# Kernel tuning notes

Hardware: AMD Instinct MI355X
Metric: run time of the kernel (lower is better)

Reference implementation:

```python
import jax, jax.numpy as jnp
import numpy as np

N = 20000      # nodes
E = 320000     # edges (before self loops)
HID = 128      # args.hidden
HEADS = 8
C1 = HID // 2  # 64, gat1 out per head -> 512 concat
C2 = HID // 4  # 32, gat2 out per head -> 256 concat
D1 = HEADS * C1  # 512
D2 = HEADS * C2  # 256
JKD = HID + D1 + D2  # 896


def _glorot(key, shape):
    fan_in, fan_out = shape[0], shape[-1]
    s = jnp.sqrt(6.0 / (fan_in + fan_out))
    return jax.random.uniform(key, shape, jnp.float32, -s, s)


def setup_inputs() -> dict:
    key = jax.random.key(0)
    ks = jax.random.split(key, 18)
    x = jax.random.normal(ks[0], (N, HID), jnp.float32)
    edge_index = jax.random.randint(ks[1], (2, E), 0, N, dtype=jnp.int32)
    return {
        "x": x,
        "edge_index": edge_index,
        # GATv2 layer 1
        "Wl1": _glorot(ks[2], (HID, D1)), "bl1": jnp.zeros((D1,), jnp.float32),
        "Wr1": _glorot(ks[3], (HID, D1)), "br1": jnp.zeros((D1,), jnp.float32),
        "att1": _glorot(ks[4], (HEADS, C1)),
        "bias1": jnp.zeros((D1,), jnp.float32),
        # GATv2 layer 2
        "Wl2": _glorot(ks[5], (D1, D2)), "bl2": jnp.zeros((D2,), jnp.float32),
        "Wr2": _glorot(ks[6], (D1, D2)), "br2": jnp.zeros((D2,), jnp.float32),
        "att2": _glorot(ks[7], (HEADS, C2)),
        "bias2": jnp.zeros((D2,), jnp.float32),
        # JK linear
        "Wjk": _glorot(ks[8], (JKD, HID)), "bjk": jnp.zeros((HID,), jnp.float32),
    }


def gatv2_layer(x, src, dst, Wl, bl, Wr, br, att, bias, n):
    """PyG GATv2Conv (concat=True, eval mode: no dropout), neg_slope=0.2."""
    H, C = att.shape
    xl = (x @ Wl + bl).reshape(n, H, C)  # source transform (messages)
    xr = (x @ Wr + br).reshape(n, H, C)  # target transform
    e = jax.nn.leaky_relu(xl[src] + xr[dst], 0.2)        # [E,H,C]
    logits = jnp.einsum('ehc,hc->eh', e, att)            # [E,H]
    # numerically stable segment softmax over incoming edges per dst node
    m = jax.ops.segment_max(logits, dst, num_segments=n) # [N,H]
    a = jnp.exp(logits - m[dst])
    denom = jax.ops.segment_sum(a, dst, num_segments=n)
    alpha = a / denom[dst]                               # [E,H]
    out = jax.ops.segment_sum(alpha[:, :, None] * xl[src], dst, num_segments=n)
    return out.reshape(n, H * C) + bias


def reference(x, edge_index, Wl1, bl1, Wr1, br1, att1, bias1,
              Wl2, bl2, Wr2, br2, att2, bias2, Wjk, bjk):
    n = x.shape[0]
    loop = jnp.arange(n, dtype=edge_index.dtype)
    src = jnp.concatenate([edge_index[0], loop])  # add self loops (PyG default)
    dst = jnp.concatenate([edge_index[1], loop])

    jk0 = x
    h1 = jax.nn.elu(gatv2_layer(x, src, dst, Wl1, bl1, Wr1, br1, att1, bias1, n))
    h2 = jax.nn.elu(gatv2_layer(h1, src, dst, Wl2, bl2, Wr2, br2, att2, bias2, n))
    jk = jnp.concatenate([jk0, h1, h2], axis=-1)  # JumpingKnowledge('cat')
    return jk @ Wjk + bjk
```

## Files before the change

kernel.cpp:

```cpp
#include <hip/hip_runtime.h>

typedef unsigned short u16;
typedef __attribute__((ext_vector_type(8))) short bf16x8;
typedef __attribute__((ext_vector_type(4))) float f32x4;

__device__ __forceinline__ float bf2f(u16 u) { return __uint_as_float(((unsigned)u) << 16); }
__device__ __forceinline__ u16 f2bf(float f) {
  unsigned u = __float_as_uint(f);
  u += 0x7fffu + ((u >> 16) & 1u);
  return (u16)(u >> 16);
}
__device__ __forceinline__ void bf2x2(unsigned w, float& lo, float& hi) {
  lo = __uint_as_float(w << 16);
  hi = __uint_as_float(w & 0xffff0000u);
}
__device__ __forceinline__ unsigned pk2(float lo, float hi) {
  return (unsigned)f2bf(lo) | ((unsigned)f2bf(hi) << 16);
}

__device__ __forceinline__ float red8(float p) {
  p += __int_as_float(__builtin_amdgcn_ds_swizzle(__float_as_int(p), 0x041F));
  p += __int_as_float(__builtin_amdgcn_ds_swizzle(__float_as_int(p), 0x081F));
  p += __int_as_float(__builtin_amdgcn_ds_swizzle(__float_as_int(p), 0x101F));
  return p;
}
__device__ __forceinline__ float red4(float p) {
  p += __int_as_float(__builtin_amdgcn_ds_swizzle(__float_as_int(p), 0x041F));
  p += __int_as_float(__builtin_amdgcn_ds_swizzle(__float_as_int(p), 0x081F));
  return p;
}

__global__ __launch_bounds__(256) void prepw_kernel(
    const float* __restrict__ x,
    const float* __restrict__ bl1, const float* __restrict__ br1,
    const float* __restrict__ bl2, const float* __restrict__ br2,
    const float* __restrict__ Wl1, const float* __restrict__ Wr1,
    const float* __restrict__ Wl2, const float* __restrict__ Wr2,
    const float* __restrict__ Wjk,
    u16* __restrict__ XH, float* __restrict__ BC1, float* __restrict__ BC2,
    int* __restrict__ cur, u16* __restrict__ Wp,
    int nx, int total, int prepBlocks)
{
  if (blockIdx.x < prepBlocks) {
    int i = blockIdx.x * 256 + threadIdx.x;
    if (i >= total) return;
    if (i < nx) { XH[i] = f2bf(x[i]); return; }
    int j = i - nx;
    if (j < 1024) { BC1[j] = (j < 512) ? bl1[j] : br1[j - 512]; return; }
    if (j < 1536) { int t = j - 1024; BC2[t] = (t < 256) ? bl2[t] : br2[t - 256]; return; }
    cur[j - 1536] = 0;
    return;
  }
  __shared__ float T[64][65];
  int t = blockIdx.x - prepBlocks;
  const float *Wa, *Wb; int Nhalf, lds, k0, n0, KsT, SUBS; size_t obase; bool split;
  if (t < 32) {
    int kt = t & 1, nt = t >> 1;
    k0 = kt * 64; n0 = nt * 64; obase = 0; KsT = 4; SUBS = 8; split = true;
    Wa = Wl1; Wb = Wr1; Nhalf = 512; lds = 512;
  } else if (t < 96) {
    int tt = t - 32; int kt = tt & 7, nt = tt >> 3;
    k0 = kt * 64; n0 = nt * 64; obase = 262144; KsT = 16; SUBS = 8; split = true;
    Wa = Wl2; Wb = Wr2; Nhalf = 256; lds = 256;
  } else {
    int tt = t - 96; int kt = tt % 14, nt = tt / 14;
    k0 = kt * 64; n0 = nt * 64; obase = 786432; KsT = 28; SUBS = 4; split = false;
    Wa = Wjk; Wb = nullptr; Nhalf = 128; lds = 128;
  }
  const int tid = threadIdx.x;
  const int lane = tid & 63, unit = tid >> 6;
  {
    int n = n0 + lane;
    const float* S = (n < Nhalf) ? Wa : Wb;
    int nn = (n < Nhalf) ? n : n - Nhalf;
#pragma unroll
    for (int r = 0; r < 16; ++r) {
      int kl = unit + 4 * r;
      T[kl][lane] = S[(size_t)(k0 + kl) * lds + nn];
    }
  }
  __syncthreads();
  const int tn = n0 >> 6;
#pragma unroll
  for (int u = 0; u < 2; ++u) {
    int c = unit * 2 + u;
    int ks_l = c >> 2, nc = c & 3;
    int ksg = (k0 >> 5) + ks_l;
    size_t ob = obase + ((size_t)(tn * KsT + ksg) * SUBS + nc) * 512 + lane * 8;
#pragma unroll
    for (int j = 0; j < 8; ++j) {
      float v = T[ks_l * 32 + (lane >> 4) * 8 + j][nc * 16 + (lane & 15)];
      u16 h = f2bf(v);
      Wp[ob + j] = h;
      if (split) Wp[ob + 2048 + j] = f2bf(v - bf2f(h));
    }
  }
}

__global__ __launch_bounds__(256) void hist_kernel(
    const int* __restrict__ ei, int E, int ET, int* __restrict__ cnt)
{
  int e = blockIdx.x * 256 + threadIdx.x;
  if (e >= ET) return;
  int d = (e < E) ? ei[E + e] : (e - E);
  atomicAdd(&cnt[d], 1);
}

__global__ __launch_bounds__(1024) void scan_kernel(
    int* __restrict__ cnt, int* __restrict__ rowptr, int n)
{
  __shared__ int wsum[16];
  __shared__ int carry;
  const int tid = threadIdx.x, lane = tid & 63, wv = tid >> 6;
  if (tid == 0) carry = 0;
  __syncthreads();
  for (int base = 0; base < n; base += 1024) {
    int i = base + tid;
    int v = (i < n) ? cnt[i] : 0;
    if (i < n) cnt[i] = 0;
    int s = v;
#pragma unroll
    for (int ofs = 1; ofs < 64; ofs <<= 1) {
      int t = __shfl_up(s, ofs);
      if (lane >= ofs) s += t;
    }
    if (lane == 63) wsum[wv] = s;
    __syncthreads();
    if (wv == 0 && lane < 16) {
      int t = wsum[lane];
#pragma unroll
      for (int ofs = 1; ofs < 16; ofs <<= 1) {
        int u = __shfl_up(t, ofs);
        if (lane >= ofs) t += u;
      }
      wsum[lane] = t;
    }
    __syncthreads();
    int waveoff = (wv == 0) ? 0 : wsum[wv - 1];
    if (i < n) rowptr[i] = carry + waveoff + s - v;
    int tot = wsum[15];
    __syncthreads();
    if (tid == 0) carry += tot;
    __syncthreads();
  }
  if (threadIdx.x == 0) rowptr[n] = carry;
}

__global__ __launch_bounds__(256) void scatter_kernel(
    const int* __restrict__ ei, int E, int ET,
    const int* __restrict__ rowptr, int* __restrict__ cur, int* __restrict__ srcs)
{
  int e = blockIdx.x * 256 + threadIdx.x;
  if (e >= ET) return;
  int s, d;
  if (e < E) { s = ei[e]; d = ei[E + e]; } else { s = e - E; d = s; }
  int pos = rowptr[d] + atomicAdd(&cur[d], 1);
  srcs[pos] = s;
}

template<int MROWS, int NW, int WPE, bool SPLIT, bool BF16OUT, int LDSU16>
__global__ __launch_bounds__(NW * 64, WPE) void gemmct_kernel(
    const u16* __restrict__ A0, int lda0, int K0,
    const u16* __restrict__ A1, int lda1, int K1,
    const u16* __restrict__ A2, int lda2, int K2,
    const u16* __restrict__ Wp, int KsT,
    int kof0, int kof1, int kof2,
    const float* __restrict__ bias,
    void* __restrict__ Cv, int ldc, int M, int N)
{
  constexpr int SUBS = SPLIT ? 8 : 4;
  __shared__ u16 ldsA[LDSU16];
  const int tid  = threadIdx.x;
  const int lane = tid & 63;
  const int wv   = tid >> 6;
  const int quad = lane >> 4;
  const int r16  = lane & 15;
  const int m0   = blockIdx.x * MROWS;

  const u16* As[3]   = {A0, A1, A2};
  const int  Ks[3]   = {K0, K1, K2};
  const int  ldas[3] = {lda0, lda1, lda2};
  const int  kofs[3] = {kof0, kof1, kof2};

  int soff[3];
  int so = 0;
#pragma unroll
  for (int s = 0; s < 3; ++s) {
    const int K = Ks[s];
    soff[s] = so;
    if (K == 0) continue;
    const int stride = K + 8;
    const int cpr = K >> 3;
    const int sh  = 32 - __clz(cpr - 1);
    const int tot = MROWS << sh;
    for (int c = tid; c < tot; c += NW * 64) {
      int row = c >> sh, kc = c & ((1 << sh) - 1);
      if (kc < cpr) {
        int sr = m0 + row; if (sr >= M) sr = M - 1;
        uint4 v = *reinterpret_cast<const uint4*>(As[s] + (size_t)sr * ldas[s] + kc * 8);
        *reinterpret_cast<uint4*>(&ldsA[so + row * stride + kc * 8]) = v;
      }
    }
    so += MROWS * stride;
  }
  __syncthreads();

  constexpr int MM = MROWS / 16;
  for (int n0w = wv * 64; n0w < N; n0w += NW * 64) {
    const int t = n0w >> 6;
    f32x4 acc[MM][4];
#pragma unroll
    for (int mm = 0; mm < MM; ++mm)
#pragma unroll
      for (int nc = 0; nc < 4; ++nc) acc[mm][nc] = (f32x4){0.f, 0.f, 0.f, 0.f};

#pragma unroll
    for (int s = 0; s < 3; ++s) {
      const int K = Ks[s];
      if (K == 0) continue;
      const int stride = K + 8;
      const int ksb = kofs[s] >> 5;
      const u16* lbase = &ldsA[soff[s] + r16 * stride + quad * 8];

#pragma unroll 2
      for (int k0 = 0; k0 < K; k0 += 32) {
        const int ks = ksb + (k0 >> 5);
        const u16* ch = Wp + (((size_t)(t * KsT + ks) * SUBS) << 9) + lane * 8;
        bf16x8 af[MM];
#pragma unroll
        for (int mm = 0; mm < MM; ++mm)
          af[mm] = *reinterpret_cast<const bf16x8*>(lbase + mm * 16 * stride + k0);
        bf16x8 whf[4], wlf[4];
#pragma unroll
        for (int nc = 0; nc < 4; ++nc) {
          whf[nc] = *reinterpret_cast<const bf16x8*>(ch + (nc << 9));
          if (SPLIT) wlf[nc] = *reinterpret_cast<const bf16x8*>(ch + ((4 + nc) << 9));
        }
#pragma unroll
        for (int mm = 0; mm < MM; ++mm)
#pragma unroll
          for (int nc = 0; nc < 4; ++nc) {
            acc[mm][nc] = __builtin_amdgcn_mfma_f32_16x16x32_bf16(whf[nc], af[mm], acc[mm][nc], 0, 0, 0);
            if (SPLIT)
              acc[mm][nc] = __builtin_amdgcn_mfma_f32_16x16x32_bf16(wlf[nc], af[mm], acc[mm][nc], 0, 0, 0);
          }
      }
    }

#pragma unroll
    for (int mm = 0; mm < MM; ++mm) {
      const int m = m0 + mm * 16 + r16;
      if (m >= M) continue;
#pragma unroll
      for (int nc = 0; nc < 4; ++nc) {
        const int n = n0w + nc * 16 + quad * 4;
        float b0 = 0.f, b1 = 0.f, b2 = 0.f, b3 = 0.f;
        if (bias) {
          float4 bv = *reinterpret_cast<const float4*>(bias + n);
          b0 = bv.x; b1 = bv.y; b2 = bv.z; b3 = bv.w;
        }
        float v0 = acc[mm][nc][0] + b0;
        float v1 = acc[mm][nc][1] + b1;
        float v2 = acc[mm][nc][2] + b2;
        float v3 = acc[mm][nc][3] + b3;
        if (BF16OUT) {
          ushort4 o = { f2bf(v0), f2bf(v1), f2bf(v2), f2bf(v3) };
          *reinterpret_cast<ushort4*>((u16*)Cv + (size_t)m * ldc + n) = o;
        } else {
          float4 o = { v0, v1, v2, v3 };
          *reinterpret_cast<float4*>((float*)Cv + (size_t)m * ldc + n) = o;
        }
      }
    }
  }
}

template<int VPL>
__device__ __forceinline__ void load_row(const u16* p, float* dst) {
  if constexpr (VPL == 8) {
    uint4 t = *reinterpret_cast<const uint4*>(p);
    bf2x2(t.x, dst[0], dst[1]); bf2x2(t.y, dst[2], dst[3]);
    bf2x2(t.z, dst[4], dst[5]); bf2x2(t.w, dst[6], dst[7]);
  } else {
    uint2 t = *reinterpret_cast<const uint2*>(p);
    bf2x2(t.x, dst[0], dst[1]); bf2x2(t.y, dst[2], dst[3]);
  }
}

__global__ __launch_bounds__(256) void gat_node1_kernel(
    const u16* __restrict__ XLR,
    const int* __restrict__ rowptr, const int* __restrict__ srcs,
    const float* __restrict__ att, const float* __restrict__ bias,
    u16* __restrict__ Hh, int Nn)
{
  constexpr int D = 512;
  constexpr int VPL = 8;
  const int lane = threadIdx.x & 63;
  const int wv  = (blockIdx.x * 256 + threadIdx.x) >> 6;
  const int nwv = (gridDim.x * 256) >> 6;

  float c1[VPL], c2[VPL], biasR[VPL];
#pragma unroll
  for (int w = 0; w < VPL; ++w) {
    float a = att[lane * VPL + w];
    c1[w] = 0.6f * a;
    c2[w] = 0.4f * a;
    biasR[w] = bias[lane * VPL + w];
  }

  for (int d = wv; d < Nn; d += nwv) {
    float xr[VPL];
    load_row<VPL>(XLR + (size_t)d * (2 * D) + D + lane * VPL, xr);

    const int jb = rowptr[d], je = rowptr[d + 1];

    float acc[VPL];
    load_row<VPL>(XLR + (size_t)srcs[jb] * (2 * D) + lane * VPL, acc);
    float p0 = 0.f;
#pragma unroll
    for (int w = 0; w < VPL; ++w) {
      float v = acc[w] + xr[w];
      p0 = fmaf(c1[w], v, fmaf(c2[w], fabsf(v), p0));
    }
    p0 = red8(p0);
    float den = 1.f;

    int j = jb + 1;
    for (; j + 5 < je; j += 6) {
      float xs[6][VPL];
      float p[6];
#pragma unroll
      for (int q = 0; q < 6; ++q)
        load_row<VPL>(XLR + (size_t)srcs[j + q] * (2 * D) + lane * VPL, xs[q]);
#pragma unroll
      for (int q = 0; q < 6; ++q) {
        float pp = 0.f;
#pragma unroll
        for (int w = 0; w < VPL; ++w) {
          float v = xs[q][w] + xr[w];
          pp = fmaf(c1[w], v, fmaf(c2[w], fabsf(v), pp));
        }
        p[q] = pp;
      }
#pragma unroll
      for (int q = 0; q < 6; ++q)
        p[q] += __int_as_float(__builtin_amdgcn_ds_swizzle(__float_as_int(p[q]), 0x041F));
#pragma unroll
      for (int q = 0; q < 6; ++q)
        p[q] += __int_as_float(__builtin_amdgcn_ds_swizzle(__float_as_int(p[q]), 0x081F));
#pragma unroll
      for (int q = 0; q < 6; ++q)
        p[q] += __int_as_float(__builtin_amdgcn_ds_swizzle(__float_as_int(p[q]), 0x101F));
      float e[6];
#pragma unroll
      for (int q = 0; q < 6; ++q) e[q] = __expf(p[q] - p0);
      den += ((e[0] + e[1]) + (e[2] + e[3])) + (e[4] + e[5]);
#pragma unroll
      for (int w = 0; w < VPL; ++w) {
        float t0 = fmaf(e[0], xs[0][w], fmaf(e[1], xs[1][w], acc[w]));
        float t1 = fmaf(e[2], xs[2][w], fmaf(e[3], xs[3][w], t0));
        acc[w] = fmaf(e[4], xs[4][w], fmaf(e[5], xs[5][w], t1));
      }
    }
    if (j + 3 < je) {
      float xs[4][VPL];
      float p[4];
#pragma unroll
      for (int q = 0; q < 4; ++q)
        load_row<VPL>(XLR + (size_t)srcs[j + q] * (2 * D) + lane * VPL, xs[q]);
#pragma unroll
      for (int q = 0; q < 4; ++q) {
        float pp = 0.f;
#pragma unroll
        for (int w = 0; w < VPL; ++w) {
          float v = xs[q][w] + xr[w];
          pp = fmaf(c1[w], v, fmaf(c2[w], fabsf(v), pp));
        }
        p[q] = pp;
      }
#pragma unroll
      for (int q = 0; q < 4; ++q)
        p[q] += __int_as_float(__builtin_amdgcn_ds_swizzle(__float_as_int(p[q]), 0x041F));
#pragma unroll
      for (int q = 0; q < 4; ++q)
        p[q] += __int_as_float(__builtin_amdgcn_ds_swizzle(__float_as_int(p[q]), 0x081F));
#pragma unroll
      for (int q = 0; q < 4; ++q)
        p[q] += __int_as_float(__builtin_amdgcn_ds_swizzle(__float_as_int(p[q]), 0x101F));
      float e[4];
#pragma unroll
      for (int q = 0; q < 4; ++q) e[q] = __expf(p[q] - p0);
      den += (e[0] + e[1]) + (e[2] + e[3]);
#pragma unroll
      for (int w = 0; w < VPL; ++w) {
        float t0 = fmaf(e[0], xs[0][w], fmaf(e[1], xs[1][w], acc[w]));
        acc[w] = fmaf(e[2], xs[2][w], fmaf(e[3], xs[3][w], t0));
      }
      j += 4;
    }
    if (j + 1 < je) {
      float xa[VPL], xb[VPL];
      load_row<VPL>(XLR + (size_t)srcs[j]     * (2 * D) + lane * VPL, xa);
      load_row<VPL>(XLR + (size_t)srcs[j + 1] * (2 * D) + lane * VPL, xb);
      float pa = 0.f, pb = 0.f;
#pragma unroll
      for (int w = 0; w < VPL; ++w) {
        float va = xa[w] + xr[w];
        float vb = xb[w] + xr[w];
        pa = fmaf(c1[w], va, fmaf(c2[w], fabsf(va), pa));
        pb = fmaf(c1[w], vb, fmaf(c2[w], fabsf(vb), pb));
      }
      pa = red8(pa); pb = red8(pb);
      const float ea = __expf(pa - p0);
      const float eb = __expf(pb - p0);
      den += ea + eb;
#pragma unroll
      for (int w = 0; w < VPL; ++w)
        acc[w] = fmaf(ea, xa[w], fmaf(eb, xb[w], acc[w]));
      j += 2;
    }
    if (j < je) {
      float xa[VPL];
      load_row<VPL>(XLR + (size_t)srcs[j] * (2 * D) + lane * VPL, xa);
      float pa = 0.f;
#pragma unroll
      for (int w = 0; w < VPL; ++w) {
        float va = xa[w] + xr[w];
        pa = fmaf(c1[w], va, fmaf(c2[w], fabsf(va), pa));
      }
      pa = red8(pa);
      const float ea = __expf(pa - p0);
      den += ea;
#pragma unroll
      for (int w = 0; w < VPL; ++w) acc[w] = fmaf(ea, xa[w], acc[w]);
    }

    const float inv = 1.f / den;
    float o[VPL];
#pragma unroll
    for (int w = 0; w < VPL; ++w) {
      float v = fmaf(acc[w], inv, biasR[w]);
      o[w] = v > 0.f ? v : (__expf(v) - 1.f);
    }
    uint4 ov = { pk2(o[0], o[1]), pk2(o[2], o[3]), pk2(o[4], o[5]), pk2(o[6], o[7]) };
    *reinterpret_cast<uint4*>(Hh + (size_t)d * D + lane * VPL) = ov;
  }
}

__global__ __launch_bounds__(256) void gat_node2_kernel(
    const u16* __restrict__ XLR,
    const int* __restrict__ rowptr, const int* __restrict__ srcs,
    const float* __restrict__ att, const float* __restrict__ bias,
    u16* __restrict__ Hh, int Nn)
{
  constexpr int D = 256;
  const int lane = threadIdx.x & 63;
  const int half = lane >> 5;
  const int l32  = lane & 31;
  const int wv  = (blockIdx.x * 256 + threadIdx.x) >> 6;
  const int nwv = (gridDim.x * 256) >> 6;

  float c1[8], c2[8], biasR[8];
#pragma unroll
  for (int w = 0; w < 8; ++w) {
    float a = att[l32 * 8 + w];
    c1[w] = 0.6f * a;
    c2[w] = 0.4f * a;
    biasR[w] = bias[l32 * 8 + w];
  }

  for (int d = wv; d < Nn; d += nwv) {
    float xr[8];
    load_row<8>(XLR + (size_t)d * (2 * D) + D + l32 * 8, xr);

    const int jb = rowptr[d], je = rowptr[d + 1];

    float acc[8];
    load_row<8>(XLR + (size_t)srcs[jb] * (2 * D) + l32 * 8, acc);
    float p0 = 0.f;
#pragma unroll
    for (int w = 0; w < 8; ++w) {
      float v = acc[w] + xr[w];
      p0 = fmaf(c1[w], v, fmaf(c2[w], fabsf(v), p0));
    }
    p0 = red4(p0);
    float den;
    if (half) {
      den = 0.f;
#pragma unroll
      for (int w = 0; w < 8; ++w) acc[w] = 0.f;
    } else {
      den = 1.f;
    }

    int j = jb + 1;
    for (; j + 7 < je; j += 8) {
      float xs[4][8];
      float p[4];
#pragma unroll
      for (int q = 0; q < 4; ++q)
        load_row<8>(XLR + (size_t)srcs[j + 2 * q + half] * (2 * D) + l32 * 8, xs[q]);
#pragma unroll
      for (int q = 0; q < 4; ++q) {
        float pp = 0.f;
#pragma unroll
        for (int w = 0; w < 8; ++w) {
          float v = xs[q][w] + xr[w];
          pp = fmaf(c1[w], v, fmaf(c2[w], fabsf(v), pp));
        }
        p[q] = pp;
      }
#pragma unroll
      for (int q = 0; q < 4; ++q)
        p[q] += __int_as_float(__builtin_amdgcn_ds_swizzle(__float_as_int(p[q]), 0x041F));
#pragma unroll
      for (int q = 0; q < 4; ++q)
        p[q] += __int_as_float(__builtin_amdgcn_ds_swizzle(__float_as_int(p[q]), 0x081F));
      float e[4];
#pragma unroll
      for (int q = 0; q < 4; ++q) e[q] = __expf(p[q] - p0);
      den += (e[0] + e[1]) + (e[2] + e[3]);
#pragma unroll
      for (int w = 0; w < 8; ++w) {
        float t0 = fmaf(e[0], xs[0][w], fmaf(e[1], xs[1][w], acc[w]));
        acc[w] = fmaf(e[2], xs[2][w], fmaf(e[3], xs[3][w], t0));
      }
    }
    for (; j < je; j += 2) {
      int jj = j + half;
      const bool valid = jj < je;
      if (!valid) jj = je - 1;
      float xa[8];
      load_row<8>(XLR + (size_t)srcs[jj] * (2 * D) + l32 * 8, xa);
      float pa = 0.f;
#pragma unroll
      for (int w = 0; w < 8; ++w) {
        float v = xa[w] + xr[w];
        pa = fmaf(c1[w], v, fmaf(c2[w], fabsf(v), pa));
      }
      pa = red4(pa);
      const float ea = valid ? __expf(pa - p0) : 0.f;
      den += ea;
#pragma unroll
      for (int w = 0; w < 8; ++w) acc[w] = fmaf(ea, xa[w], acc[w]);
    }

    den += __shfl_xor(den, 32);
#pragma unroll
    for (int w = 0; w < 8; ++w) acc[w] += __shfl_xor(acc[w], 32);

    if (half == 0) {
      const float inv = 1.f / den;
      float o[8];
#pragma unroll
      for (int w = 0; w < 8; ++w) {
        float v = fmaf(acc[w], inv, biasR[w]);
        o[w] = v > 0.f ? v : (__expf(v) - 1.f);
      }
      uint4 ov = { pk2(o[0], o[1]), pk2(o[2], o[3]), pk2(o[4], o[5]), pk2(o[6], o[7]) };
      *reinterpret_cast<uint4*>(Hh + (size_t)d * D + l32 * 8) = ov;
    }
  }
}


extern "C" void kernel_launch(void* const* d_in, const int* in_sizes, int n_in,
                              void* d_out, int out_size, void* d_ws, size_t ws_size,
                              hipStream_t stream) {
  const float* x     = (const float*)d_in[0];
  const int*   ei    = (const int*)d_in[1];
  const float* Wl1   = (const float*)d_in[2];
  const float* bl1   = (const float*)d_in[3];
  const float* Wr1   = (const float*)d_in[4];
  const float* br1   = (const float*)d_in[5];
  const float* att1  = (const float*)d_in[6];
  const float* bias1 = (const float*)d_in[7];
  const float* Wl2   = (const float*)d_in[8];
  const float* bl2   = (const float*)d_in[9];
  const float* Wr2   = (const float*)d_in[10];
  const float* br2   = (const float*)d_in[11];
  const float* att2  = (const float*)d_in[12];
  const float* bias2 = (const float*)d_in[13];
  const float* Wjk   = (const float*)d_in[14];
  const float* bjk   = (const float*)d_in[15];
  float* out = (float*)d_out;

  const int Nn = in_sizes[0] / 128;
  const int E  = in_sizes[1] / 2;
  const int ET = E + Nn;

  const size_t nx = (size_t)Nn * 128;

  const size_t oW1  = 0;
  const size_t oW2  = 262144;
  const size_t oWjk = 786432;
  const size_t npack = 901120;

  char* ws = (char*)d_ws;
  size_t off = 0;
  u16* XH = (u16*)(ws + off); off += nx * 2;
  u16* Wp = (u16*)(ws + off); off += npack * 2;
  float* BC1 = (float*)(ws + off); off += 1024 * 4;
  float* BC2 = (float*)(ws + off); off += 512 * 4;
  u16* XLR1 = (u16*)(ws + off);
  u16* XLR2 = XLR1;
  off += (size_t)Nn * 1024 * 2;
  u16* H1h = (u16*)(ws + off); off += (size_t)Nn * 512 * 2;
  u16* H2h = (u16*)(ws + off); off += (size_t)Nn * 256 * 2;
  int* rowptr = (int*)(ws + off); off += (size_t)(Nn + 1) * 4;
  int* cur    = (int*)(ws + off); off += (size_t)Nn * 4;
  int* srcs   = (int*)(ws + off); off += (size_t)ET * 4;

  const int nodeblocks = 5000;

  const int nprep = (int)(nx + 1536 + Nn);
  const int prepBlocks = (nprep + 255) / 256;
  prepw_kernel<<<prepBlocks + 124, 256, 0, stream>>>(
      x, bl1, br1, bl2, br2, Wl1, Wr1, Wl2, Wr2, Wjk,
      XH, BC1, BC2, cur, Wp, (int)nx, nprep, prepBlocks);
  hist_kernel<<<(ET + 255) / 256, 256, 0, stream>>>(ei, E, ET, cur);
  scan_kernel<<<1, 1024, 0, stream>>>(cur, rowptr, Nn);
  scatter_kernel<<<(ET + 255) / 256, 256, 0, stream>>>(ei, E, ET, rowptr, cur, srcs);

  gemmct_kernel<32, 8, 4, true, true, 32 * 136>
      <<<(Nn + 31) / 32, 512, 0, stream>>>(
      XH, 128, 128, nullptr, 0, 0, nullptr, 0, 0,
      Wp + oW1, 4, 0, 0, 0, BC1,
      XLR1, 1024, Nn, 1024);
  gat_node1_kernel<<<nodeblocks, 256, 0, stream>>>(
      XLR1, rowptr, srcs, att1, bias1, H1h, Nn);

  gemmct_kernel<48, 8, 4, true, true, 48 * 520>
      <<<(Nn + 47) / 48, 512, 0, stream>>>(
      H1h, 512, 512, nullptr, 0, 0, nullptr, 0, 0,
      Wp + oW2, 16, 0, 0, 0, BC2,
      XLR2, 512, Nn, 512);
  gat_node2_kernel<<<nodeblocks, 256, 0, stream>>>(
      XLR2, rowptr, srcs, att2, bias2, H2h, Nn);

  gemmct_kernel<16, 2, 1, false, false, 16 * 920>
      <<<(Nn + 15) / 16, 128, 0, stream>>>(
      XH, 128, 128, H1h, 512, 512, H2h, 256, 256,
      Wp + oWjk, 28, 0, 128, 640, bjk,
      out, 128, Nn, 128);
}
```

Baseline: 320.3 us.

## Fuse scatter into GEMM1 launch and double-buffer gathers in GAT node kernels

The CSR scatter is merged into the first GEMM launch as extra blocks, so the two independent pieces of work share one grid and one kernel launch is removed. In both GAT aggregation kernels, the main edge loop now uses ping-pong register buffers, issuing the next group of neighbour-row gathers before computing on the current group to hide gather latency. The double buffering raises register pressure and may lower occupancy. The scatter blocks in the fused kernel also run with a 512-thread block shape and carry the GEMM's LDS allocation.

```diff
diff --git a/kernel.cpp b/kernel.cpp
--- a/kernel.cpp
+++ b/kernel.cpp
@@ -16,18 +16,6 @@
 }
 __device__ __forceinline__ unsigned pk2(float lo, float hi) {
   return (unsigned)f2bf(lo) | ((unsigned)f2bf(hi) << 16);
-}
-
-__device__ __forceinline__ float red8(float p) {
-  p += __int_as_float(__builtin_amdgcn_ds_swizzle(__float_as_int(p), 0x041F));
-  p += __int_as_float(__builtin_amdgcn_ds_swizzle(__float_as_int(p), 0x081F));
-  p += __int_as_float(__builtin_amdgcn_ds_swizzle(__float_as_int(p), 0x101F));
-  return p;
-}
-__device__ __forceinline__ float red4(float p) {
-  p += __int_as_float(__builtin_amdgcn_ds_swizzle(__float_as_int(p), 0x041F));
-  p += __int_as_float(__builtin_amdgcn_ds_swizzle(__float_as_int(p), 0x081F));
-  return p;
 }
 
 __global__ __launch_bounds__(256) void prepw_kernel(
@@ -146,20 +134,9 @@
   if (threadIdx.x == 0) rowptr[n] = carry;
 }
 
-__global__ __launch_bounds__(256) void scatter_kernel(
-    const int* __restrict__ ei, int E, int ET,
-    const int* __restrict__ rowptr, int* __restrict__ cur, int* __restrict__ srcs)
-{
-  int e = blockIdx.x * 256 + threadIdx.x;
-  if (e >= ET) return;
-  int s, d;
-  if (e < E) { s = ei[e]; d = ei[E + e]; } else { s = e - E; d = s; }
-  int pos = rowptr[d] + atomicAdd(&cur[d], 1);
-  srcs[pos] = s;
-}
-
-template<int MROWS, int NW, int WPE, bool SPLIT, bool BF16OUT, int LDSU16>
-__global__ __launch_bounds__(NW * 64, WPE) void gemmct_kernel(
+template<int MROWS, int NW, bool SPLIT, bool BF16OUT>
+__device__ __forceinline__ void gemmct_body(
+    u16* __restrict__ ldsA, int bid,
     const u16* __restrict__ A0, int lda0, int K0,
     const u16* __restrict__ A1, int lda1, int K1,
     const u16* __restrict__ A2, int lda2, int K2,
@@ -169,13 +146,12 @@
     void* __restrict__ Cv, int ldc, int M, int N)
 {
   constexpr int SUBS = SPLIT ? 8 : 4;
-  __shared__ u16 ldsA[LDSU16];
   const int tid  = threadIdx.x;
   const int lane = tid & 63;
   const int wv   = tid >> 6;
   const int quad = lane >> 4;
   const int r16  = lane & 15;
-  const int m0   = blockIdx.x * MROWS;
+  const int m0   = bid * MROWS;
 
   const u16* As[3]   = {A0, A1, A2};
   const int  Ks[3]   = {K0, K1, K2};
@@ -275,6 +251,46 @@
   }
 }
 
+template<int MROWS, int NW, int WPE, bool SPLIT, bool BF16OUT, int LDSU16>
+__global__ __launch_bounds__(NW * 64, WPE) void gemmct_kernel(
+    const u16* __restrict__ A0, int lda0, int K0,
+    const u16* __restrict__ A1, int lda1, int K1,
+    const u16* __restrict__ A2, int lda2, int K2,
+    const u16* __restrict__ Wp, int KsT,
+    int kof0, int kof1, int kof2,
+    const float* __restrict__ bias,
+    void* __restrict__ Cv, int ldc, int M, int N)
+{
+  __shared__ u16 ldsA[LDSU16];
+  gemmct_body<MROWS, NW, SPLIT, BF16OUT>(
+      ldsA, blockIdx.x, A0, lda0, K0, A1, lda1, K1, A2, lda2, K2,
+      Wp, KsT, kof0, kof1, kof2, bias, Cv, ldc, M, N);
+}
+
+template<int MROWS, int NW, int WPE, bool SPLIT, bool BF16OUT, int LDSU16>
+__global__ __launch_bounds__(NW * 64, WPE) void gemm1_scatter_kernel(
+    const u16* __restrict__ A0, int lda0, int K0,
+    const u16* __restrict__ Wp, int KsT,
+    const float* __restrict__ bias,
+    void* __restrict__ Cv, int ldc, int M, int N, int gemmBlocks,
+    const int* __restrict__ ei, int E, int ET,
+    const int* __restrict__ rowptr, int* __restrict__ cur, int* __restrict__ srcs)
+{
+  __shared__ u16 ldsA[LDSU16];
+  if ((int)blockIdx.x < gemmBlocks) {
+    gemmct_body<MROWS, NW, SPLIT, BF16OUT>(
+        ldsA, blockIdx.x, A0, lda0, K0, nullptr, 0, 0, nullptr, 0, 0,
+        Wp, KsT, 0, 0, 0, bias, Cv, ldc, M, N);
+    return;
+  }
+  int e = ((int)blockIdx.x - gemmBlocks) * (NW * 64) + (int)threadIdx.x;
+  if (e >= ET) return;
+  int s, d;
+  if (e < E) { s = ei[e]; d = ei[E + e]; } else { s = e - E; d = s; }
+  int pos = rowptr[d] + atomicAdd(&cur[d], 1);
+  srcs[pos] = s;
+}
+
 template<int VPL>
 __device__ __forceinline__ void load_row(const u16* p, float* dst) {
   if constexpr (VPL == 8) {
@@ -287,6 +303,52 @@
   }
 }
 
+__device__ __forceinline__ void g1_load6(
+    const u16* __restrict__ XLR, const int* __restrict__ srcs,
+    int j, int laneoff, float xs[6][8])
+{
+#pragma unroll
+  for (int q = 0; q < 6; ++q)
+    load_row<8>(XLR + (size_t)srcs[j + q] * 1024 + laneoff, xs[q]);
+}
+
+__device__ __forceinline__ void g1_compute6(
+    const float xs[6][8], const float xr[8],
+    const float c1[8], const float c2[8],
+    float p0, float& den, float acc[8])
+{
+  float p[6];
+#pragma unroll
+  for (int q = 0; q < 6; ++q) {
+    float pp = 0.f;
+#pragma unroll
+    for (int w = 0; w < 8; ++w) {
+      float v = xs[q][w] + xr[w];
+      pp = fmaf(c1[w], v, fmaf(c2[w], fabsf(v), pp));
+    }
+    p[q] = pp;
+  }
+#pragma unroll
+  for (int q = 0; q < 6; ++q)
+    p[q] += __int_as_float(__builtin_amdgcn_ds_swizzle(__float_as_int(p[q]), 0x041F));
+#pragma unroll
+  for (int q = 0; q < 6; ++q)
+    p[q] += __int_as_float(__builtin_amdgcn_ds_swizzle(__float_as_int(p[q]), 0x081F));
+#pragma unroll
+  for (int q = 0; q < 6; ++q)
+    p[q] += __int_as_float(__builtin_amdgcn_ds_swizzle(__float_as_int(p[q]), 0x101F));
+  float e[6];
+#pragma unroll
+  for (int q = 0; q < 6; ++q) e[q] = __expf(p[q] - p0);
+  den += ((e[0] + e[1]) + (e[2] + e[3])) + (e[4] + e[5]);
+#pragma unroll
+  for (int w = 0; w < 8; ++w) {
+    float t0 = fmaf(e[0], xs[0][w], fmaf(e[1], xs[1][w], acc[w]));
+    float t1 = fmaf(e[2], xs[2][w], fmaf(e[3], xs[3][w], t0));
+    acc[w] = fmaf(e[4], xs[4][w], fmaf(e[5], xs[5][w], t1));
+  }
+}
+
 __global__ __launch_bounds__(256) void gat_node1_kernel(
     const u16* __restrict__ XLR,
     const int* __restrict__ rowptr, const int* __restrict__ srcs,
@@ -296,44 +358,62 @@
   constexpr int D = 512;
   constexpr int VPL = 8;
   const int lane = threadIdx.x & 63;
+  const int laneoff = lane * VPL;
   const int wv  = (blockIdx.x * 256 + threadIdx.x) >> 6;
   const int nwv = (gridDim.x * 256) >> 6;
 
   float c1[VPL], c2[VPL], biasR[VPL];
 #pragma unroll
   for (int w = 0; w < VPL; ++w) {
-    float a = att[lane * VPL + w];
+    float a = att[laneoff + w];
     c1[w] = 0.6f * a;
     c2[w] = 0.4f * a;
-    biasR[w] = bias[lane * VPL + w];
+    biasR[w] = bias[laneoff + w];
   }
 
   for (int d = wv; d < Nn; d += nwv) {
     float xr[VPL];
-    load_row<VPL>(XLR + (size_t)d * (2 * D) + D + lane * VPL, xr);
+    load_row<VPL>(XLR + (size_t)d * (2 * D) + D + laneoff, xr);
 
     const int jb = rowptr[d], je = rowptr[d + 1];
 
     float acc[VPL];
-    load_row<VPL>(XLR + (size_t)srcs[jb] * (2 * D) + lane * VPL, acc);
+    load_row<VPL>(XLR + (size_t)srcs[jb] * (2 * D) + laneoff, acc);
     float p0 = 0.f;
 #pragma unroll
     for (int w = 0; w < VPL; ++w) {
       float v = acc[w] + xr[w];
       p0 = fmaf(c1[w], v, fmaf(c2[w], fabsf(v), p0));
     }
-    p0 = red8(p0);
+    p0 += __int_as_float(__builtin_amdgcn_ds_swizzle(__float_as_int(p0), 0x041F));
+    p0 += __int_as_float(__builtin_amdgcn_ds_swizzle(__float_as_int(p0), 0x081F));
+    p0 += __int_as_float(__builtin_amdgcn_ds_swizzle(__float_as_int(p0), 0x101F));
     float den = 1.f;
 
     int j = jb + 1;
-    for (; j + 5 < je; j += 6) {
-      float xs[6][VPL];
-      float p[6];
-#pragma unroll
-      for (int q = 0; q < 6; ++q)
-        load_row<VPL>(XLR + (size_t)srcs[j + q] * (2 * D) + lane * VPL, xs[q]);
-#pragma unroll
-      for (int q = 0; q < 6; ++q) {
+    if (j + 5 < je) {
+      float xs[6][VPL], ys[6][VPL];
+      g1_load6(XLR, srcs, j, laneoff, xs);
+      j += 6;
+      for (;;) {
+        bool haveY = (j + 5 < je);
+        if (haveY) { g1_load6(XLR, srcs, j, laneoff, ys); j += 6; }
+        g1_compute6(xs, xr, c1, c2, p0, den, acc);
+        if (!haveY) break;
+        bool haveX = (j + 5 < je);
+        if (haveX) { g1_load6(XLR, srcs, j, laneoff, xs); j += 6; }
+        g1_compute6(ys, xr, c1, c2, p0, den, acc);
+        if (!haveX) break;
+      }
+    }
+    if (j + 3 < je) {
+      float xs[4][VPL];
+      float p[4];
+#pragma unroll
+      for (int q = 0; q < 4; ++q)
+        load_row<VPL>(XLR + (size_t)srcs[j + q] * (2 * D) + laneoff, xs[q]);
+#pragma unroll
+      for (int q = 0; q < 4; ++q) {
         float pp = 0.f;
 #pragma unroll
         for (int w = 0; w < VPL; ++w) {
@@ -343,42 +423,6 @@
         p[q] = pp;
       }
 #pragma unroll
-      for (int q = 0; q < 6; ++q)
-        p[q] += __int_as_float(__builtin_amdgcn_ds_swizzle(__float_as_int(p[q]), 0x041F));
-#pragma unroll
-      for (int q = 0; q < 6; ++q)
-        p[q] += __int_as_float(__builtin_amdgcn_ds_swizzle(__float_as_int(p[q]), 0x081F));
-#pragma unroll
-      for (int q = 0; q < 6; ++q)
-        p[q] += __int_as_float(__builtin_amdgcn_ds_swizzle(__float_as_int(p[q]), 0x101F));
-      float e[6];
-#pragma unroll
-      for (int q = 0; q < 6; ++q) e[q] = __expf(p[q] - p0);
-      den += ((e[0] + e[1]) + (e[2] + e[3])) + (e[4] + e[5]);
-#pragma unroll
-      for (int w = 0; w < VPL; ++w) {
-        float t0 = fmaf(e[0], xs[0][w], fmaf(e[1], xs[1][w], acc[w]));
-        float t1 = fmaf(e[2], xs[2][w], fmaf(e[3], xs[3][w], t0));
-        acc[w] = fmaf(e[4], xs[4][w], fmaf(e[5], xs[5][w], t1));
-      }
-    }
-    if (j + 3 < je) {
-      float xs[4][VPL];
-      float p[4];
-#pragma unroll
-      for (int q = 0; q < 4; ++q)
-        load_row<VPL>(XLR + (size_t)srcs[j + q] * (2 * D) + lane * VPL, xs[q]);
-#pragma unroll
-      for (int q = 0; q < 4; ++q) {
-        float pp = 0.f;
-#pragma unroll
-        for (int w = 0; w < VPL; ++w) {
-          float v = xs[q][w] + xr[w];
-          pp = fmaf(c1[w], v, fmaf(c2[w], fabsf(v), pp));
-        }
-        p[q] = pp;
-      }
-#pragma unroll
       for (int q = 0; q < 4; ++q)
         p[q] += __int_as_float(__builtin_amdgcn_ds_swizzle(__float_as_int(p[q]), 0x041F));
 #pragma unroll
@@ -400,8 +444,8 @@
     }
     if (j + 1 < je) {
       float xa[VPL], xb[VPL];
-      load_row<VPL>(XLR + (size_t)srcs[j]     * (2 * D) + lane * VPL, xa);
-      load_row<VPL>(XLR + (size_t)srcs[j + 1] * (2 * D) + lane * VPL, xb);
+      load_row<VPL>(XLR + (size_t)srcs[j]     * (2 * D) + laneoff, xa);
+      load_row<VPL>(XLR + (size_t)srcs[j + 1] * (2 * D) + laneoff, xb);
       float pa = 0.f, pb = 0.f;
 #pragma unroll
       for (int w = 0; w < VPL; ++w) {
@@ -410,7 +454,12 @@
         pa = fmaf(c1[w], va, fmaf(c2[w], fabsf(va), pa));
         pb = fmaf(c1[w], vb, fmaf(c2[w], fabsf(vb), pb));
       }
-      pa = red8(pa); pb = red8(pb);
+      pa += __int_as_float(__builtin_amdgcn_ds_swizzle(__float_as_int(pa), 0x041F));
+      pb += __int_as_float(__builtin_amdgcn_ds_swizzle(__float_as_int(pb), 0x041F));
+      pa += __int_as_float(__builtin_amdgcn_ds_swizzle(__float_as_int(pa), 0x081F));
+      pb += __int_as_float(__builtin_amdgcn_ds_swizzle(__float_as_int(pb), 0x081F));
+      pa += __int_as_float(__builtin_amdgcn_ds_swizzle(__float_as_int(pa), 0x101F));
+      pb += __int_as_float(__builtin_amdgcn_ds_swizzle(__float_as_int(pb), 0x101F));
       const float ea = __expf(pa - p0);
       const float eb = __expf(pb - p0);
       den += ea + eb;
@@ -421,14 +470,16 @@
     }
     if (j < je) {
       float xa[VPL];
-      load_row<VPL>(XLR + (size_t)srcs[j] * (2 * D) + lane * VPL, xa);
+      load_row<VPL>(XLR + (size_t)srcs[j] * (2 * D) + laneoff, xa);
       float pa = 0.f;
 #pragma unroll
       for (int w = 0; w < VPL; ++w) {
         float va = xa[w] + xr[w];
         pa = fmaf(c1[w], va, fmaf(c2[w], fabsf(va), pa));
       }
-      pa = red8(pa);
+      pa += __int_as_float(__builtin_amdgcn_ds_swizzle(__float_as_int(pa), 0x041F));
+      pa += __int_as_float(__builtin_amdgcn_ds_swizzle(__float_as_int(pa), 0x081F));
+      pa += __int_as_float(__builtin_amdgcn_ds_swizzle(__float_as_int(pa), 0x101F));
       const float ea = __expf(pa - p0);
       den += ea;
 #pragma unroll
@@ -443,7 +494,49 @@
       o[w] = v > 0.f ? v : (__expf(v) - 1.f);
     }
     uint4 ov = { pk2(o[0], o[1]), pk2(o[2], o[3]), pk2(o[4], o[5]), pk2(o[6], o[7]) };
-    *reinterpret_cast<uint4*>(Hh + (size_t)d * D + lane * VPL) = ov;
+    *reinterpret_cast<uint4*>(Hh + (size_t)d * D + laneoff) = ov;
+  }
+}
+
+__device__ __forceinline__ void g2_load4(
+    const u16* __restrict__ XLR, const int* __restrict__ srcs,
+    int j, int half, int l32off, float xs[4][8])
+{
+#pragma unroll
+  for (int q = 0; q < 4; ++q)
+    load_row<8>(XLR + (size_t)srcs[j + 2 * q + half] * 512 + l32off, xs[q]);
+}
+
+__device__ __forceinline__ void g2_compute4(
+    const float xs[4][8], const float xr[8],
+    const float c1[8], const float c2[8],
+    float p0, float& den, float acc[8])
+{
+  float p[4];
+#pragma unroll
+  for (int q = 0; q < 4; ++q) {
+    float pp = 0.f;
+#pragma unroll
+    for (int w = 0; w < 8; ++w) {
+      float v = xs[q][w] + xr[w];
+      pp = fmaf(c1[w], v, fmaf(c2[w], fabsf(v), pp));
+    }
+    p[q] = pp;
+  }
+#pragma unroll
+  for (int q = 0; q < 4; ++q)
+    p[q] += __int_as_float(__builtin_amdgcn_ds_swizzle(__float_as_int(p[q]), 0x041F));
+#pragma unroll
+  for (int q = 0; q < 4; ++q)
+    p[q] += __int_as_float(__builtin_amdgcn_ds_swizzle(__float_as_int(p[q]), 0x081F));
+  float e[4];
+#pragma unroll
+  for (int q = 0; q < 4; ++q) e[q] = __expf(p[q] - p0);
+  den += (e[0] + e[1]) + (e[2] + e[3]);
+#pragma unroll
+  for (int w = 0; w < 8; ++w) {
+    float t0 = fmaf(e[0], xs[0][w], fmaf(e[1], xs[1][w], acc[w]));
+    acc[w] = fmaf(e[2], xs[2][w], fmaf(e[3], xs[3][w], t0));
   }
 }
 
@@ -457,33 +550,35 @@
   const int lane = threadIdx.x & 63;
   const int half = lane >> 5;
   const int l32  = lane & 31;
+  const int l32off = l32 * 8;
   const int wv  = (blockIdx.x * 256 + threadIdx.x) >> 6;
   const int nwv = (gridDim.x * 256) >> 6;
 
   float c1[8], c2[8], biasR[8];
 #pragma unroll
   for (int w = 0; w < 8; ++w) {
-    float a = att[l32 * 8 + w];
+    float a = att[l32off + w];
     c1[w] = 0.6f * a;
     c2[w] = 0.4f * a;
-    biasR[w] = bias[l32 * 8 + w];
+    biasR[w] = bias[l32off + w];
   }
 
   for (int d = wv; d < Nn; d += nwv) {
     float xr[8];
-    load_row<8>(XLR + (size_t)d * (2 * D) + D + l32 * 8, xr);
+    load_row<8>(XLR + (size_t)d * (2 * D) + D + l32off, xr);
 
     const int jb = rowptr[d], je = rowptr[d + 1];
 
     float acc[8];
-    load_row<8>(XLR + (size_t)srcs[jb] * (2 * D) + l32 * 8, acc);
+    load_row<8>(XLR + (size_t)srcs[jb] * (2 * D) + l32off, acc);
     float p0 = 0.f;
 #pragma unroll
     for (int w = 0; w < 8; ++w) {
       float v = acc[w] + xr[w];
       p0 = fmaf(c1[w], v, fmaf(c2[w], fabsf(v), p0));
     }
-    p0 = red4(p0);
+    p0 += __int_as_float(__builtin_amdgcn_ds_swizzle(__float_as_int(p0), 0x041F));
+    p0 += __int_as_float(__builtin_amdgcn_ds_swizzle(__float_as_int(p0), 0x081F));
     float den;
     if (half) {
       den = 0.f;
@@ -494,36 +589,19 @@
     }
 
     int j = jb + 1;
-    for (; j + 7 < je; j += 8) {
-      float xs[4][8];
-      float p[4];
-#pragma unroll
-      for (int q = 0; q < 4; ++q)
-        load_row<8>(XLR + (size_t)srcs[j + 2 * q + half] * (2 * D) + l32 * 8, xs[q]);
-#pragma unroll
-      for (int q = 0; q < 4; ++q) {
-        float pp = 0.f;
-#pragma unroll
-        for (int w = 0; w < 8; ++w) {
-          float v = xs[q][w] + xr[w];
-          pp = fmaf(c1[w], v, fmaf(c2[w], fabsf(v), pp));
-        }
-        p[q] = pp;
-      }
-#pragma unroll
-      for (int q = 0; q < 4; ++q)
-        p[q] += __int_as_float(__builtin_amdgcn_ds_swizzle(__float_as_int(p[q]), 0x041F));
-#pragma unroll
-      for (int q = 0; q < 4; ++q)
-        p[q] += __int_as_float(__builtin_amdgcn_ds_swizzle(__float_as_int(p[q]), 0x081F));
-      float e[4];
-#pragma unroll
-      for (int q = 0; q < 4; ++q) e[q] = __expf(p[q] - p0);
-      den += (e[0] + e[1]) + (e[2] + e[3]);
-#pragma unroll
-      for (int w = 0; w < 8; ++w) {
-        float t0 = fmaf(e[0], xs[0][w], fmaf(e[1], xs[1][w], acc[w]));
-        acc[w] = fmaf(e[2], xs[2][w], fmaf(e[3], xs[3][w], t0));
+    if (j + 7 < je) {
+      float xs[4][8], ys[4][8];
+      g2_load4(XLR, srcs, j, half, l32off, xs);
+      j += 8;
+      for (;;) {
+        bool haveY = (j + 7 < je);
+        if (haveY) { g2_load4(XLR, srcs, j, half, l32off, ys); j += 8; }
+        g2_compute4(xs, xr, c1, c2, p0, den, acc);
+        if (!haveY) break;
+        bool haveX = (j + 7 < je);
+        if (haveX) { g2_load4(XLR, srcs, j, half, l32off, xs); j += 8; }
+        g2_compute4(ys, xr, c1, c2, p0, den, acc);
+        if (!haveX) break;
       }
     }
     for (; j < je; j += 2) {
@@ -531,14 +609,15 @@
       const bool valid = jj < je;
       if (!valid) jj = je - 1;
       float xa[8];
-      load_row<8>(XLR + (size_t)srcs[jj] * (2 * D) + l32 * 8, xa);
+      load_row<8>(XLR + (size_t)srcs[jj] * (2 * D) + l32off, xa);
       float pa = 0.f;
 #pragma unroll
       for (int w = 0; w < 8; ++w) {
         float v = xa[w] + xr[w];
         pa = fmaf(c1[w], v, fmaf(c2[w], fabsf(v), pa));
       }
-      pa = red4(pa);
+      pa += __int_as_float(__builtin_amdgcn_ds_swizzle(__float_as_int(pa), 0x041F));
+      pa += __int_as_float(__builtin_amdgcn_ds_swizzle(__float_as_int(pa), 0x081F));
       const float ea = valid ? __expf(pa - p0) : 0.f;
       den += ea;
 #pragma unroll
@@ -558,7 +637,7 @@
         o[w] = v > 0.f ? v : (__expf(v) - 1.f);
       }
       uint4 ov = { pk2(o[0], o[1]), pk2(o[2], o[3]), pk2(o[4], o[5]), pk2(o[6], o[7]) };
-      *reinterpret_cast<uint4*>(Hh + (size_t)d * D + l32 * 8) = ov;
+      *reinterpret_cast<uint4*>(Hh + (size_t)d * D + l32off) = ov;
     }
   }
 }
@@ -620,13 +699,15 @@
       XH, BC1, BC2, cur, Wp, (int)nx, nprep, prepBlocks);
   hist_kernel<<<(ET + 255) / 256, 256, 0, stream>>>(ei, E, ET, cur);
   scan_kernel<<<1, 1024, 0, stream>>>(cur, rowptr, Nn);
-  scatter_kernel<<<(ET + 255) / 256, 256, 0, stream>>>(ei, E, ET, rowptr, cur, srcs);
-
-  gemmct_kernel<32, 8, 4, true, true, 32 * 136>
-      <<<(Nn + 31) / 32, 512, 0, stream>>>(
-      XH, 128, 128, nullptr, 0, 0, nullptr, 0, 0,
-      Wp + oW1, 4, 0, 0, 0, BC1,
-      XLR1, 1024, Nn, 1024);
+
+  const int g1blocks = (Nn + 31) / 32;
+  const int scatBlocks = (ET + 511) / 512;
+  gemm1_scatter_kernel<32, 8, 4, true, true, 32 * 136>
+      <<<g1blocks + scatBlocks, 512, 0, stream>>>(
+      XH, 128, 128,
+      Wp + oW1, 4, BC1,
+      XLR1, 1024, Nn, 1024, g1blocks,
+      ei, E, ET, rowptr, cur, srcs);
   gat_node1_kernel<<<nodeblocks, 256, 0, stream>>>(
       XLR1, rowptr, srcs, att1, bias1, H1h, Nn);
 
```

Measured after the change: 308.0 us. 3.9% less time.
